# Kernel optimization log

Measured on AMD Instinct MI355X. Metric: run time of the kernel, lower is better.

## Reference

```python
import jax, jax.numpy as jnp
import numpy as np

N_NODES = 50000
N_EDGES = 800000
IN_DIM = 128
HIDDEN = 32
HEADS = 4
OUT_DIM = 40
NEG_SLOPE = 0.2


def _segment_softmax(logits, seg, num_segments):
    # logits: [E, H], seg: [E] destination node ids
    m = jax.ops.segment_max(logits, seg, num_segments=num_segments)  # [N, H]
    e = jnp.exp(logits - m[seg])
    s = jax.ops.segment_sum(e, seg, num_segments=num_segments)  # [N, H]
    return e / s[seg]


def _gat_conv(x, src, dst, W, a_src, a_dst, b, heads, out_ch, concat):
    N = x.shape[0]
    h = (x @ W).reshape(N, heads, out_ch)  # [N, H, C]
    alpha_src = jnp.einsum('nhc,hc->nh', h, a_src)  # [N, H]
    alpha_dst = jnp.einsum('nhc,hc->nh', h, a_dst)  # [N, H]
    logits = jax.nn.leaky_relu(alpha_src[src] + alpha_dst[dst], NEG_SLOPE)  # [E, H]
    alpha = _segment_softmax(logits, dst, N)  # [E, H]
    msg = h[src] * alpha[:, :, None]  # [E, H, C]
    out = jax.ops.segment_sum(msg, dst, num_segments=N)  # [N, H, C]
    if concat:
        out = out.reshape(N, heads * out_ch)
    else:
        out = out.mean(axis=1)
    return out + b


def setup_inputs() -> dict:
    key = jax.random.key(0)
    ks = jax.random.split(key, 12)
    x = jax.random.normal(ks[0], (N_NODES, IN_DIM), dtype=jnp.float32)
    edge_index = jax.random.randint(ks[1], (2, N_EDGES), 0, N_NODES, dtype=jnp.int64 if jax.config.read('jax_enable_x64') else jnp.int32)
    s1 = 1.0 / np.sqrt(IN_DIM)
    W1 = jax.random.uniform(ks[2], (IN_DIM, HEADS * HIDDEN), jnp.float32, -s1, s1)
    att_src1 = jax.random.uniform(ks[3], (HEADS, HIDDEN), jnp.float32, -1, 1) / np.sqrt(HIDDEN)
    att_dst1 = jax.random.uniform(ks[4], (HEADS, HIDDEN), jnp.float32, -1, 1) / np.sqrt(HIDDEN)
    b1 = jnp.zeros((HEADS * HIDDEN,), jnp.float32)
    s2 = 1.0 / np.sqrt(HEADS * HIDDEN)
    W2 = jax.random.uniform(ks[5], (HEADS * HIDDEN, OUT_DIM), jnp.float32, -s2, s2)
    att_src2 = jax.random.uniform(ks[6], (1, OUT_DIM), jnp.float32, -1, 1) / np.sqrt(OUT_DIM)
    att_dst2 = jax.random.uniform(ks[7], (1, OUT_DIM), jnp.float32, -1, 1) / np.sqrt(OUT_DIM)
    b2 = jnp.zeros((OUT_DIM,), jnp.float32)
    return {
        'x': x, 'edge_index': edge_index,
        'W1': W1, 'att_src1': att_src1, 'att_dst1': att_dst1, 'b1': b1,
        'W2': W2, 'att_src2': att_src2, 'att_dst2': att_dst2, 'b2': b2,
    }


def reference(x, edge_index, W1, att_src1, att_dst1, b1, W2, att_src2, att_dst2, b2):
    N = x.shape[0]
    # PyG GATConv default add_self_loops=True
    loop = jnp.arange(N, dtype=edge_index.dtype)
    src = jnp.concatenate([edge_index[0], loop])
    dst = jnp.concatenate([edge_index[1], loop])
    # dropout(p=0.6) is identity in eval mode
    h = _gat_conv(x, src, dst, W1, att_src1, att_dst1, b1, HEADS, HIDDEN, concat=True)
    h = jax.nn.relu(h)
    out = _gat_conv(h, src, dst, W2, att_src2, att_dst2, b2, 1, OUT_DIM, concat=True)
    return out
```

## Files before the change

kernel.cpp:

```cpp
#include <hip/hip_runtime.h>
#include <hip/hip_bf16.h>
#include <hip/hip_fp16.h>
#include <math.h>

#define N_NODES 50000
#define N_EDGES 800000
#define E_TOT   850000
#define IN_DIM  128
#define HID     32
#define HEADS   4
#define D1      128
#define OUT_DIM 40
#define H2P     64
#define NEG_SLOPE 0.2f

#define SCAN_TILE 1024
#define SCAN_NB   ((N_NODES + SCAN_TILE - 1) / SCAN_TILE)
#define G1_ROWS   64
#define GEMM1_NB  ((N_NODES + G1_ROWS - 1) / G1_ROWS)
#define CNT_NB    ((E_TOT + 255) / 256)
#define W2T_LD    132

__global__ __launch_bounds__(256) void gemm1_count(
    const float* __restrict__ x, const float* __restrict__ W,
    const float* __restrict__ as_v, const float* __restrict__ ad_v,
    __half* __restrict__ h1h, float* __restrict__ asrc, float* __restrict__ adst,
    const int* __restrict__ ei, int* __restrict__ deg)
{
  __shared__ float xs[G1_ROWS][IN_DIM];
  __shared__ float wbuf[2][8 * D1];
  const int t = threadIdx.x;
  if (blockIdx.x >= GEMM1_NB) {
    int e = (blockIdx.x - GEMM1_NB) * 256 + t;
    if (e < E_TOT) {
      int d = (e < N_EDGES) ? ei[N_EDGES + e] : e - N_EDGES;
      atomicAdd(deg + d, 1);
    }
    return;
  }
  const int nb = blockIdx.x * G1_ROWS;
  for (int i = t; i < G1_ROWS * (IN_DIM / 4); i += 256) {
    int r = i >> 5, k4 = (i & 31) * 4;
    int n = nb + r;
    float4 v = (n < N_NODES) ? *reinterpret_cast<const float4*>(x + (size_t)n * IN_DIM + k4)
                             : make_float4(0.f, 0.f, 0.f, 0.f);
    *reinterpret_cast<float4*>(&xs[r][k4]) = v;
  }
  float4 wreg = *reinterpret_cast<const float4*>(W + t * 4);
  *reinterpret_cast<float4*>(&wbuf[0][t * 4]) = wreg;
  __syncthreads();

  const int ct = t & 31, col0 = ct * 4;
  const int rt = t >> 5;
  float acc[8][4];
#pragma unroll
  for (int r = 0; r < 8; ++r)
#pragma unroll
    for (int c = 0; c < 4; ++c) acc[r][c] = 0.f;

  const int NK8 = IN_DIM / 8;
  for (int k8 = 0; k8 < NK8; ++k8) {
    const int cur = k8 & 1;
    if (k8 + 1 < NK8)
      wreg = *reinterpret_cast<const float4*>(W + (size_t)(k8 + 1) * 8 * D1 + t * 4);
#pragma unroll
    for (int half = 0; half < 2; ++half) {
      const int kb = k8 * 8 + half * 4;
      float4 xv[8];
#pragma unroll
      for (int r = 0; r < 8; ++r)
        xv[r] = *reinterpret_cast<const float4*>(&xs[rt * 8 + r][kb]);
      float4 wv[4];
#pragma unroll
      for (int kk = 0; kk < 4; ++kk)
        wv[kk] = *reinterpret_cast<const float4*>(&wbuf[cur][(half * 4 + kk) * D1 + col0]);
#pragma unroll
      for (int r = 0; r < 8; ++r) {
        acc[r][0] += xv[r].x * wv[0].x + xv[r].y * wv[1].x + xv[r].z * wv[2].x + xv[r].w * wv[3].x;
        acc[r][1] += xv[r].x * wv[0].y + xv[r].y * wv[1].y + xv[r].z * wv[2].y + xv[r].w * wv[3].y;
        acc[r][2] += xv[r].x * wv[0].z + xv[r].y * wv[1].z + xv[r].z * wv[2].z + xv[r].w * wv[3].z;
        acc[r][3] += xv[r].x * wv[0].w + xv[r].y * wv[1].w + xv[r].z * wv[2].w + xv[r].w * wv[3].w;
      }
    }
    if (k8 + 1 < NK8)
      *reinterpret_cast<float4*>(&wbuf[cur ^ 1][t * 4]) = wreg;
    __syncthreads();
  }

  const int head = col0 >> 5;
  const int cc0  = col0 & 31;
  const float4 asv = *reinterpret_cast<const float4*>(as_v + head * HID + cc0);
  const float4 adv = *reinterpret_cast<const float4*>(ad_v + head * HID + cc0);
#pragma unroll
  for (int r = 0; r < 8; ++r) {
    int n = nb + rt * 8 + r;
    bool ok = n < N_NODES;
    if (ok) {
      __half2 p0 = __floats2half2_rn(acc[r][0], acc[r][1]);
      __half2 p1 = __floats2half2_rn(acc[r][2], acc[r][3]);
      uint2 pk;
      pk.x = *reinterpret_cast<unsigned*>(&p0);
      pk.y = *reinterpret_cast<unsigned*>(&p1);
      *reinterpret_cast<uint2*>(h1h + (size_t)n * D1 + col0) = pk;
    }
    float cs = acc[r][0] * asv.x + acc[r][1] * asv.y + acc[r][2] * asv.z + acc[r][3] * asv.w;
    float cd = acc[r][0] * adv.x + acc[r][1] * adv.y + acc[r][2] * adv.z + acc[r][3] * adv.w;
#pragma unroll
    for (int off = 1; off < 8; off <<= 1) {
      cs += __shfl_xor(cs, off, 64);
      cd += __shfl_xor(cd, off, 64);
    }
    if ((ct & 7) == 0 && ok) {
      asrc[n * HEADS + head] = cs;
      adst[n * HEADS + head] = cd;
    }
  }
}

__global__ void zero_deg(int* __restrict__ deg)
{
  int i = blockIdx.x * blockDim.x + threadIdx.x;
  if (i < N_NODES) deg[i] = 0;
}

__global__ __launch_bounds__(256) void scan_p1(const int* __restrict__ deg,
                                               int* __restrict__ blocksum)
{
  int base = blockIdx.x * SCAN_TILE + threadIdx.x * 4;
  int s = 0;
#pragma unroll
  for (int i = 0; i < 4; ++i) {
    int idx = base + i;
    if (idx < N_NODES) s += deg[idx];
  }
#pragma unroll
  for (int off = 1; off < 64; off <<= 1) s += __shfl_xor(s, off, 64);
  __shared__ int ws[4];
  if ((threadIdx.x & 63) == 0) ws[threadIdx.x >> 6] = s;
  __syncthreads();
  if (threadIdx.x == 0) blocksum[blockIdx.x] = ws[0] + ws[1] + ws[2] + ws[3];
}

__global__ void scan_p2(const int* __restrict__ blocksum, int* __restrict__ blockoff,
                        int* __restrict__ row_off)
{
  int t = threadIdx.x;
  int v = (t < SCAN_NB) ? blocksum[t] : 0;
  int incl = v;
#pragma unroll
  for (int off = 1; off < 64; off <<= 1) {
    int u = __shfl_up(incl, off, 64);
    if (t >= off) incl += u;
  }
  if (t < SCAN_NB) blockoff[t] = incl - v;
  if (t == 0) row_off[N_NODES] = E_TOT;
}

__global__ __launch_bounds__(256) void scan_p3(const int* __restrict__ deg,
                                               const int* __restrict__ blockoff,
                                               int* __restrict__ row_off,
                                               int* __restrict__ cursor)
{
  const int t = threadIdx.x;
  const int lane = t & 63, wid = t >> 6;
  int base = blockIdx.x * SCAN_TILE + t * 4;
  int local[4]; int lsum = 0;
#pragma unroll
  for (int i = 0; i < 4; ++i) {
    int idx = base + i;
    local[i] = (idx < N_NODES) ? deg[idx] : 0;
    lsum += local[i];
  }
  int incl = lsum;
#pragma unroll
  for (int off = 1; off < 64; off <<= 1) {
    int u = __shfl_up(incl, off, 64);
    if (lane >= off) incl += u;
  }
  __shared__ int wtot[4];
  if (lane == 63) wtot[wid] = incl;
  __syncthreads();
  int wpre = 0;
  for (int w = 0; w < wid; ++w) wpre += wtot[w];
  int run = blockoff[blockIdx.x] + wpre + (incl - lsum);
#pragma unroll
  for (int i = 0; i < 4; ++i) {
    int idx = base + i;
    if (idx < N_NODES) { row_off[idx] = run; cursor[idx] = run; run += local[i]; }
  }
}

__global__ void scatter_csr(const int* __restrict__ ei, int* __restrict__ cursor,
                            int* __restrict__ csr_src)
{
  int e = blockIdx.x * blockDim.x + threadIdx.x;
  if (e >= E_TOT) return;
  int s, d;
  if (e < N_EDGES) { s = ei[e]; d = ei[N_EDGES + e]; }
  else             { s = d = e - N_EDGES; }
  int pos = atomicAdd(cursor + d, 1);
  csr_src[pos] = s;
}

__global__ __launch_bounds__(256) void agg1(
    const int* __restrict__ row_off, const int* __restrict__ csr_src,
    const float* __restrict__ asrc, const float* __restrict__ adst,
    const __half* __restrict__ h1h, const float* __restrict__ b1,
    float* __restrict__ lbuf, float* __restrict__ z)
{
  int n = blockIdx.x * 4 + (threadIdx.x >> 6);
  if (n >= N_NODES) return;
  const int lane = threadIdx.x & 63;
  const int start = row_off[n], end = row_off[n + 1];
  const int h = lane & 3;
  const float adst_h = adst[n * HEADS + h];
  float vmax = -1e30f;
  for (int i = start + (lane >> 2); i < end; i += 16)
    vmax = fmaxf(vmax, asrc[csr_src[i] * HEADS + h]);
#pragma unroll
  for (int off = 4; off < 64; off <<= 1)
    vmax = fmaxf(vmax, __shfl_xor(vmax, off, 64));
  float v = vmax + adst_h;
  const float mle = v > 0.f ? v : NEG_SLOPE * v;
  float ssum = 0.f;
  for (int i = start + (lane >> 2); i < end; i += 16) {
    float tv = asrc[csr_src[i] * HEADS + h] + adst_h;
    float le = tv > 0.f ? tv : NEG_SLOPE * tv;
    float e = __expf(le - mle);
    lbuf[(size_t)i * 4 + h] = e;
    ssum += e;
  }
#pragma unroll
  for (int off = 4; off < 64; off <<= 1)
    ssum += __shfl_xor(ssum, off, 64);
  const int hh = lane >> 4;
  const float inv = 1.f / __shfl(ssum, hh, 64);
  float2 acc = make_float2(0.f, 0.f);
  int i = start;
  for (; i + 8 <= end; i += 8) {
    float cc[8]; float2 vv[8];
#pragma unroll
    for (int u = 0; u < 8; ++u) {
      int s = csr_src[i + u];
      cc[u] = lbuf[(size_t)(i + u) * 4 + hh];
      vv[u] = __half22float2(*(reinterpret_cast<const __half2*>(h1h + (size_t)s * D1) + lane));
    }
#pragma unroll
    for (int u = 0; u < 8; ++u) {
      acc.x += cc[u] * vv[u].x;
      acc.y += cc[u] * vv[u].y;
    }
  }
  for (; i < end; ++i) {
    int s = csr_src[i];
    float c = lbuf[(size_t)i * 4 + hh];
    float2 hv = __half22float2(*(reinterpret_cast<const __half2*>(h1h + (size_t)s * D1) + lane));
    acc.x += c * hv.x;
    acc.y += c * hv.y;
  }
  float2 bb = *reinterpret_cast<const float2*>(b1 + 2 * lane);
  float r0 = acc.x * inv + bb.x;
  float r1 = acc.y * inv + bb.y;
  float2 o = make_float2(r0 > 0.f ? r0 : 0.f, r1 > 0.f ? r1 : 0.f);
  *reinterpret_cast<float2*>(z + (size_t)n * D1 + 2 * lane) = o;
}

__global__ __launch_bounds__(256) void gemm2(
    const float* __restrict__ z, const float* __restrict__ W2,
    const float* __restrict__ as2, const float* __restrict__ ad2,
    __half* __restrict__ h2h, float* __restrict__ asrc2, float* __restrict__ adst2)
{
  __shared__ float zs[32][IN_DIM];
  __shared__ float w2t[OUT_DIM][W2T_LD];
  const int nb = blockIdx.x * 32;
  const int t  = threadIdx.x;
  for (int i = t; i < 32 * (IN_DIM / 4); i += 256) {
    int r = i >> 5, k4 = (i & 31) * 4;
    int n = nb + r;
    float4 v = (n < N_NODES) ? *reinterpret_cast<const float4*>(z + (size_t)n * IN_DIM + k4)
                             : make_float4(0.f, 0.f, 0.f, 0.f);
    *reinterpret_cast<float4*>(&zs[r][k4]) = v;
  }
  for (int i = t; i < IN_DIM * OUT_DIM; i += 256) {
    int k = i / OUT_DIM, c = i - k * OUT_DIM;
    w2t[c][k] = W2[i];
  }
  __syncthreads();
  const int col = t & 63;
  const int rbase = (t >> 6) * 8;
  const bool valid = col < OUT_DIM;
  const int colc = valid ? col : (OUT_DIM - 1);
  float acc[8];
#pragma unroll
  for (int r = 0; r < 8; ++r) acc[r] = 0.f;
  for (int k = 0; k < IN_DIM; k += 4) {
    float4 wv = *reinterpret_cast<const float4*>(&w2t[colc][k]);
    float4 xv[8];
#pragma unroll
    for (int r = 0; r < 8; ++r)
      xv[r] = *reinterpret_cast<const float4*>(&zs[rbase + r][k]);
#pragma unroll
    for (int r = 0; r < 8; ++r)
      acc[r] += xv[r].x * wv.x + xv[r].y * wv.y + xv[r].z * wv.z + xv[r].w * wv.w;
  }
  const float a_s = valid ? as2[col] : 0.f;
  const float a_d = valid ? ad2[col] : 0.f;
#pragma unroll
  for (int r = 0; r < 8; ++r) {
    int n = nb + rbase + r;
    float cs = acc[r] * a_s, cd = acc[r] * a_d;
#pragma unroll
    for (int off = 32; off >= 1; off >>= 1) {
      cs += __shfl_xor(cs, off, 64);
      cd += __shfl_xor(cd, off, 64);
    }
    if (n < N_NODES) {
      if (valid) h2h[(size_t)n * H2P + col] = __float2half_rn(acc[r]);
      if (col == 0) { asrc2[n] = cs; adst2[n] = cd; }
    }
  }
}

__global__ __launch_bounds__(256) void agg2(
    const int* __restrict__ row_off, const int* __restrict__ csr_src,
    const float* __restrict__ asrc, const float* __restrict__ adst,
    const __half* __restrict__ h2h, const float* __restrict__ b2,
    float* __restrict__ lbuf, float* __restrict__ out)
{
  int n = blockIdx.x * 4 + (threadIdx.x >> 6);
  if (n >= N_NODES) return;
  const int lane = threadIdx.x & 63;
  const int start = row_off[n], end = row_off[n + 1];
  const float adstn = adst[n];
  float vmax = -1e30f;
  for (int i = start + lane; i < end; i += 64)
    vmax = fmaxf(vmax, asrc[csr_src[i]]);
#pragma unroll
  for (int off = 1; off < 64; off <<= 1)
    vmax = fmaxf(vmax, __shfl_xor(vmax, off, 64));
  float v = vmax + adstn;
  const float mle = v > 0.f ? v : NEG_SLOPE * v;
  float ssum = 0.f;
  for (int i = start + lane; i < end; i += 64) {
    float t = asrc[csr_src[i]] + adstn;
    float le = t > 0.f ? t : NEG_SLOPE * t;
    float e = __expf(le - mle);
    lbuf[i] = e;
    ssum += e;
  }
#pragma unroll
  for (int off = 1; off < 64; off <<= 1)
    ssum += __shfl_xor(ssum, off, 64);
  const float inv = 1.f / ssum;
  if (lane < OUT_DIM) {
    float acc = 0.f;
    int i = start;
    for (; i + 8 <= end; i += 8) {
      float cc[8]; float vv[8];
#pragma unroll
      for (int u = 0; u < 8; ++u) {
        cc[u] = lbuf[i + u];
        vv[u] = __half2float(h2h[(size_t)csr_src[i + u] * H2P + lane]);
      }
#pragma unroll
      for (int u = 0; u < 8; ++u) acc += cc[u] * vv[u];
    }
    for (; i < end; ++i)
      acc += lbuf[i] * __half2float(h2h[(size_t)csr_src[i] * H2P + lane]);
    out[(size_t)n * OUT_DIM + lane] = acc * inv + b2[lane];
  }
}

extern "C" void kernel_launch(void* const* d_in, const int* in_sizes, int n_in,
                              void* d_out, int out_size, void* d_ws, size_t ws_size,
                              hipStream_t stream)
{
  const float* x    = (const float*)d_in[0];
  const int*   ei   = (const int*)  d_in[1];
  const float* W1   = (const float*)d_in[2];
  const float* as1  = (const float*)d_in[3];
  const float* ad1  = (const float*)d_in[4];
  const float* b1   = (const float*)d_in[5];
  const float* W2   = (const float*)d_in[6];
  const float* as2  = (const float*)d_in[7];
  const float* ad2  = (const float*)d_in[8];
  const float* b2   = (const float*)d_in[9];
  float* out = (float*)d_out;

  float* ws = (float*)d_ws;
  __half* h1h  = (__half*)(ws + 0);
  __half* h2h  = (__half*)(ws + 0);
  float* z     = ws +  6400000;
  float* asrc1 = ws + 12800000;
  float* adst1 = ws + 13000000;
  float* asrc2 = ws + 13200000;
  float* adst2 = ws + 13250000;
  int* deg     = (int*)(ws + 13300000);
  int* row_off = (int*)(ws + 13350000);
  int* cursor  = (int*)(ws + 13410000);
  int* csr_src = (int*)(ws + 13460000);
  int* blocksum= (int*)(ws + 14320000);
  int* blockoff= (int*)(ws + 14320100);
  float* lbuf  = ws + 14400000;

  const int B = 256;
  zero_deg<<<(N_NODES + B - 1) / B, B, 0, stream>>>(deg);
  gemm1_count<<<GEMM1_NB + CNT_NB, B, 0, stream>>>(x, W1, as1, ad1, h1h, asrc1, adst1, ei, deg);
  scan_p1<<<SCAN_NB, B, 0, stream>>>(deg, blocksum);
  scan_p2<<<1, 64, 0, stream>>>(blocksum, blockoff, row_off);
  scan_p3<<<SCAN_NB, B, 0, stream>>>(deg, blockoff, row_off, cursor);
  scatter_csr<<<(E_TOT + B - 1) / B, B, 0, stream>>>(ei, cursor, csr_src);
  agg1<<<(N_NODES + 3) / 4, B, 0, stream>>>(row_off, csr_src, asrc1, adst1, h1h, b1, lbuf, z);
  gemm2<<<(N_NODES + 31) / 32, B, 0, stream>>>(z, W2, as2, ad2, h2h, asrc2, adst2);
  agg2<<<(N_NODES + 3) / 4, B, 0, stream>>>(row_off, csr_src, asrc2, adst2, h2h, b2, lbuf, out);
}
```

Before: 329.8 us.

## Use MFMA fp16 for first GEMM and keep softmax weights in LDS

Replaces the scalar-FMA first-layer GEMM with MFMA 16x16x32 fp16 instructions, using a pre-swizzled fp16 copy of W1 built in a new init kernel that also zeros degrees. The degree count now runs as a grid-stride loop inside the GEMM blocks. Both aggregation kernels keep per-edge softmax coefficients in shared memory when a node's degree fits a cap, falling back to the global buffer otherwise. This trades fp16 rounding of x inputs and extra LDS use for less FMA work and less global round-trip traffic.

```diff
diff --git a/kernel.cpp b/kernel.cpp
--- a/kernel.cpp
+++ b/kernel.cpp
@@ -13,114 +13,104 @@
 #define OUT_DIM 40
 #define H2P     64
 #define NEG_SLOPE 0.2f
+#define CAP     96
 
 #define SCAN_TILE 1024
 #define SCAN_NB   ((N_NODES + SCAN_TILE - 1) / SCAN_TILE)
-#define G1_ROWS   64
-#define GEMM1_NB  ((N_NODES + G1_ROWS - 1) / G1_ROWS)
-#define CNT_NB    ((E_TOT + 255) / 256)
+#define GEMM1_NB  ((N_NODES + 63) / 64)
 #define W2T_LD    132
 
-__global__ __launch_bounds__(256) void gemm1_count(
-    const float* __restrict__ x, const float* __restrict__ W,
+typedef _Float16 f16x8 __attribute__((ext_vector_type(8)));
+typedef float    f32x4 __attribute__((ext_vector_type(4)));
+
+__global__ __launch_bounds__(256) void init_wf_deg(
+    const float* __restrict__ W, _Float16* __restrict__ wf, int* __restrict__ deg)
+{
+  const int b = blockIdx.x, t = threadIdx.x;
+  if (b < 64) {
+    int tid = b * 256 + t;
+    int j = tid & 7, lane = (tid >> 3) & 63, nt = (tid >> 9) & 7, kc = tid >> 12;
+    int k = kc * 32 + ((lane >> 4) << 3) + j;
+    int n = nt * 16 + (lane & 15);
+    wf[tid] = (_Float16)W[k * D1 + n];
+  } else {
+    int i = (b - 64) * 256 + t;
+    if (i < N_NODES) deg[i] = 0;
+  }
+}
+
+__global__ __launch_bounds__(256) void gemm1_mfma_count(
+    const float* __restrict__ x, const _Float16* __restrict__ wf,
     const float* __restrict__ as_v, const float* __restrict__ ad_v,
-    __half* __restrict__ h1h, float* __restrict__ asrc, float* __restrict__ adst,
+    _Float16* __restrict__ h1h, float* __restrict__ asrc, float* __restrict__ adst,
     const int* __restrict__ ei, int* __restrict__ deg)
 {
-  __shared__ float xs[G1_ROWS][IN_DIM];
-  __shared__ float wbuf[2][8 * D1];
   const int t = threadIdx.x;
-  if (blockIdx.x >= GEMM1_NB) {
-    int e = (blockIdx.x - GEMM1_NB) * 256 + t;
-    if (e < E_TOT) {
-      int d = (e < N_EDGES) ? ei[N_EDGES + e] : e - N_EDGES;
-      atomicAdd(deg + d, 1);
-    }
-    return;
-  }
-  const int nb = blockIdx.x * G1_ROWS;
-  for (int i = t; i < G1_ROWS * (IN_DIM / 4); i += 256) {
-    int r = i >> 5, k4 = (i & 31) * 4;
-    int n = nb + r;
-    float4 v = (n < N_NODES) ? *reinterpret_cast<const float4*>(x + (size_t)n * IN_DIM + k4)
-                             : make_float4(0.f, 0.f, 0.f, 0.f);
-    *reinterpret_cast<float4*>(&xs[r][k4]) = v;
-  }
-  float4 wreg = *reinterpret_cast<const float4*>(W + t * 4);
-  *reinterpret_cast<float4*>(&wbuf[0][t * 4]) = wreg;
-  __syncthreads();
-
-  const int ct = t & 31, col0 = ct * 4;
-  const int rt = t >> 5;
-  float acc[8][4];
-#pragma unroll
-  for (int r = 0; r < 8; ++r)
-#pragma unroll
-    for (int c = 0; c < 4; ++c) acc[r][c] = 0.f;
-
-  const int NK8 = IN_DIM / 8;
-  for (int k8 = 0; k8 < NK8; ++k8) {
-    const int cur = k8 & 1;
-    if (k8 + 1 < NK8)
-      wreg = *reinterpret_cast<const float4*>(W + (size_t)(k8 + 1) * 8 * D1 + t * 4);
-#pragma unroll
-    for (int half = 0; half < 2; ++half) {
-      const int kb = k8 * 8 + half * 4;
-      float4 xv[8];
-#pragma unroll
-      for (int r = 0; r < 8; ++r)
-        xv[r] = *reinterpret_cast<const float4*>(&xs[rt * 8 + r][kb]);
-      float4 wv[4];
-#pragma unroll
-      for (int kk = 0; kk < 4; ++kk)
-        wv[kk] = *reinterpret_cast<const float4*>(&wbuf[cur][(half * 4 + kk) * D1 + col0]);
-#pragma unroll
-      for (int r = 0; r < 8; ++r) {
-        acc[r][0] += xv[r].x * wv[0].x + xv[r].y * wv[1].x + xv[r].z * wv[2].x + xv[r].w * wv[3].x;
-        acc[r][1] += xv[r].x * wv[0].y + xv[r].y * wv[1].y + xv[r].z * wv[2].y + xv[r].w * wv[3].y;
-        acc[r][2] += xv[r].x * wv[0].z + xv[r].y * wv[1].z + xv[r].z * wv[2].z + xv[r].w * wv[3].z;
-        acc[r][3] += xv[r].x * wv[0].w + xv[r].y * wv[1].w + xv[r].z * wv[2].w + xv[r].w * wv[3].w;
+  const int wave = t >> 6, lane = t & 63;
+  const int lr = lane & 15, lq = lane >> 4;
+  const int rowbase = blockIdx.x * 64 + wave * 16;
+  const int arow = rowbase + lr;
+
+  f32x4 acc[8];
+#pragma unroll
+  for (int nt = 0; nt < 8; ++nt) acc[nt] = (f32x4){0.f, 0.f, 0.f, 0.f};
+
+  const float* xrow = x + (size_t)arow * IN_DIM;
+  const f16x8* wfv = reinterpret_cast<const f16x8*>(wf);
+#pragma unroll
+  for (int kc = 0; kc < 4; ++kc) {
+    float4 lo = make_float4(0.f, 0.f, 0.f, 0.f), hi = lo;
+    if (arow < N_NODES) {
+      lo = *reinterpret_cast<const float4*>(xrow + kc * 32 + lq * 8);
+      hi = *reinterpret_cast<const float4*>(xrow + kc * 32 + lq * 8 + 4);
+    }
+    f16x8 a;
+    a[0] = (_Float16)lo.x; a[1] = (_Float16)lo.y; a[2] = (_Float16)lo.z; a[3] = (_Float16)lo.w;
+    a[4] = (_Float16)hi.x; a[5] = (_Float16)hi.y; a[6] = (_Float16)hi.z; a[7] = (_Float16)hi.w;
+    const f16x8* bbase = wfv + (size_t)(kc * 8) * 64 + lane;
+#pragma unroll
+    for (int nt = 0; nt < 8; ++nt) {
+      f16x8 bfrag = bbase[nt * 64];
+      acc[nt] = __builtin_amdgcn_mfma_f32_16x16x32_f16(a, bfrag, acc[nt], 0, 0, 0);
+    }
+  }
+
+  float as_lo[4], as_hi[4], ad_lo[4], ad_hi[4];
+#pragma unroll
+  for (int h = 0; h < 4; ++h) {
+    as_lo[h] = as_v[h * HID + lr];      ad_lo[h] = ad_v[h * HID + lr];
+    as_hi[h] = as_v[h * HID + 16 + lr]; ad_hi[h] = ad_v[h * HID + 16 + lr];
+  }
+#pragma unroll
+  for (int nt = 0; nt < 8; ++nt) {
+#pragma unroll
+    for (int r = 0; r < 4; ++r) {
+      int m = rowbase + lq * 4 + r;
+      if (m < N_NODES) h1h[(size_t)m * D1 + nt * 16 + lr] = (_Float16)acc[nt][r];
+    }
+  }
+#pragma unroll
+  for (int h = 0; h < 4; ++h) {
+#pragma unroll
+    for (int r = 0; r < 4; ++r) {
+      float ps = acc[2 * h][r] * as_lo[h] + acc[2 * h + 1][r] * as_hi[h];
+      float pd = acc[2 * h][r] * ad_lo[h] + acc[2 * h + 1][r] * ad_hi[h];
+#pragma unroll
+      for (int off = 1; off < 16; off <<= 1) {
+        ps += __shfl_xor(ps, off, 64);
+        pd += __shfl_xor(pd, off, 64);
       }
-    }
-    if (k8 + 1 < NK8)
-      *reinterpret_cast<float4*>(&wbuf[cur ^ 1][t * 4]) = wreg;
-    __syncthreads();
-  }
-
-  const int head = col0 >> 5;
-  const int cc0  = col0 & 31;
-  const float4 asv = *reinterpret_cast<const float4*>(as_v + head * HID + cc0);
-  const float4 adv = *reinterpret_cast<const float4*>(ad_v + head * HID + cc0);
-#pragma unroll
-  for (int r = 0; r < 8; ++r) {
-    int n = nb + rt * 8 + r;
-    bool ok = n < N_NODES;
-    if (ok) {
-      __half2 p0 = __floats2half2_rn(acc[r][0], acc[r][1]);
-      __half2 p1 = __floats2half2_rn(acc[r][2], acc[r][3]);
-      uint2 pk;
-      pk.x = *reinterpret_cast<unsigned*>(&p0);
-      pk.y = *reinterpret_cast<unsigned*>(&p1);
-      *reinterpret_cast<uint2*>(h1h + (size_t)n * D1 + col0) = pk;
-    }
-    float cs = acc[r][0] * asv.x + acc[r][1] * asv.y + acc[r][2] * asv.z + acc[r][3] * asv.w;
-    float cd = acc[r][0] * adv.x + acc[r][1] * adv.y + acc[r][2] * adv.z + acc[r][3] * adv.w;
-#pragma unroll
-    for (int off = 1; off < 8; off <<= 1) {
-      cs += __shfl_xor(cs, off, 64);
-      cd += __shfl_xor(cd, off, 64);
-    }
-    if ((ct & 7) == 0 && ok) {
-      asrc[n * HEADS + head] = cs;
-      adst[n * HEADS + head] = cd;
-    }
-  }
-}
-
-__global__ void zero_deg(int* __restrict__ deg)
-{
-  int i = blockIdx.x * blockDim.x + threadIdx.x;
-  if (i < N_NODES) deg[i] = 0;
+      int m = rowbase + lq * 4 + r;
+      if (lr == 0 && m < N_NODES) {
+        asrc[m * HEADS + h] = ps;
+        adst[m * HEADS + h] = pd;
+      }
+    }
+  }
+  for (int e = blockIdx.x * 256 + t; e < E_TOT; e += gridDim.x * 256) {
+    int d = (e < N_EDGES) ? ei[N_EDGES + e] : e - N_EDGES;
+    atomicAdd(deg + d, 1);
+  }
 }
 
 __global__ __launch_bounds__(256) void scan_p1(const int* __restrict__ deg,
@@ -208,10 +198,14 @@
     const __half* __restrict__ h1h, const float* __restrict__ b1,
     float* __restrict__ lbuf, float* __restrict__ z)
 {
-  int n = blockIdx.x * 4 + (threadIdx.x >> 6);
+  __shared__ float cbuf[4][CAP * 4];
+  const int w = threadIdx.x >> 6;
+  int n = blockIdx.x * 4 + w;
   if (n >= N_NODES) return;
   const int lane = threadIdx.x & 63;
   const int start = row_off[n], end = row_off[n + 1];
+  const bool useL = (end - start) <= CAP;
+  float* cb = cbuf[w];
   const int h = lane & 3;
   const float adst_h = adst[n * HEADS + h];
   float vmax = -1e30f;
@@ -227,7 +221,8 @@
     float tv = asrc[csr_src[i] * HEADS + h] + adst_h;
     float le = tv > 0.f ? tv : NEG_SLOPE * tv;
     float e = __expf(le - mle);
-    lbuf[(size_t)i * 4 + h] = e;
+    if (useL) cb[(i - start) * 4 + h] = e;
+    else      lbuf[(size_t)i * 4 + h] = e;
     ssum += e;
   }
 #pragma unroll
@@ -236,27 +231,37 @@
   const int hh = lane >> 4;
   const float inv = 1.f / __shfl(ssum, hh, 64);
   float2 acc = make_float2(0.f, 0.f);
-  int i = start;
-  for (; i + 8 <= end; i += 8) {
-    float cc[8]; float2 vv[8];
-#pragma unroll
-    for (int u = 0; u < 8; ++u) {
-      int s = csr_src[i + u];
-      cc[u] = lbuf[(size_t)(i + u) * 4 + hh];
-      vv[u] = __half22float2(*(reinterpret_cast<const __half2*>(h1h + (size_t)s * D1) + lane));
-    }
-#pragma unroll
-    for (int u = 0; u < 8; ++u) {
-      acc.x += cc[u] * vv[u].x;
-      acc.y += cc[u] * vv[u].y;
-    }
-  }
-  for (; i < end; ++i) {
-    int s = csr_src[i];
-    float c = lbuf[(size_t)i * 4 + hh];
-    float2 hv = __half22float2(*(reinterpret_cast<const __half2*>(h1h + (size_t)s * D1) + lane));
-    acc.x += c * hv.x;
-    acc.y += c * hv.y;
+  if (useL) {
+    int i = start;
+    for (; i + 8 <= end; i += 8) {
+      float cc[8]; float2 vv[8];
+#pragma unroll
+      for (int u = 0; u < 8; ++u) {
+        int s = csr_src[i + u];
+        cc[u] = cb[(i + u - start) * 4 + hh];
+        vv[u] = __half22float2(*(reinterpret_cast<const __half2*>(h1h + (size_t)s * D1) + lane));
+      }
+#pragma unroll
+      for (int u = 0; u < 8; ++u) {
+        acc.x += cc[u] * vv[u].x;
+        acc.y += cc[u] * vv[u].y;
+      }
+    }
+    for (; i < end; ++i) {
+      int s = csr_src[i];
+      float c = cb[(i - start) * 4 + hh];
+      float2 hv = __half22float2(*(reinterpret_cast<const __half2*>(h1h + (size_t)s * D1) + lane));
+      acc.x += c * hv.x;
+      acc.y += c * hv.y;
+    }
+  } else {
+    for (int i = start; i < end; ++i) {
+      int s = csr_src[i];
+      float c = lbuf[(size_t)i * 4 + hh];
+      float2 hv = __half22float2(*(reinterpret_cast<const __half2*>(h1h + (size_t)s * D1) + lane));
+      acc.x += c * hv.x;
+      acc.y += c * hv.y;
+    }
   }
   float2 bb = *reinterpret_cast<const float2*>(b1 + 2 * lane);
   float r0 = acc.x * inv + bb.x;
@@ -327,10 +332,14 @@
     const __half* __restrict__ h2h, const float* __restrict__ b2,
     float* __restrict__ lbuf, float* __restrict__ out)
 {
-  int n = blockIdx.x * 4 + (threadIdx.x >> 6);
+  __shared__ float cbuf[4][CAP];
+  const int w = threadIdx.x >> 6;
+  int n = blockIdx.x * 4 + w;
   if (n >= N_NODES) return;
   const int lane = threadIdx.x & 63;
   const int start = row_off[n], end = row_off[n + 1];
+  const bool useL = (end - start) <= CAP;
+  float* cb = cbuf[w];
   const float adstn = adst[n];
   float vmax = -1e30f;
   for (int i = start + lane; i < end; i += 64)
@@ -345,7 +354,8 @@
     float t = asrc[csr_src[i]] + adstn;
     float le = t > 0.f ? t : NEG_SLOPE * t;
     float e = __expf(le - mle);
-    lbuf[i] = e;
+    if (useL) cb[i - start] = e;
+    else      lbuf[i] = e;
     ssum += e;
   }
 #pragma unroll
@@ -354,19 +364,24 @@
   const float inv = 1.f / ssum;
   if (lane < OUT_DIM) {
     float acc = 0.f;
-    int i = start;
-    for (; i + 8 <= end; i += 8) {
-      float cc[8]; float vv[8];
-#pragma unroll
-      for (int u = 0; u < 8; ++u) {
-        cc[u] = lbuf[i + u];
-        vv[u] = __half2float(h2h[(size_t)csr_src[i + u] * H2P + lane]);
+    if (useL) {
+      int i = start;
+      for (; i + 8 <= end; i += 8) {
+        float cc[8]; float vv[8];
+#pragma unroll
+        for (int u = 0; u < 8; ++u) {
+          cc[u] = cb[i + u - start];
+          vv[u] = __half2float(h2h[(size_t)csr_src[i + u] * H2P + lane]);
+        }
+#pragma unroll
+        for (int u = 0; u < 8; ++u) acc += cc[u] * vv[u];
       }
-#pragma unroll
-      for (int u = 0; u < 8; ++u) acc += cc[u] * vv[u];
-    }
-    for (; i < end; ++i)
-      acc += lbuf[i] * __half2float(h2h[(size_t)csr_src[i] * H2P + lane]);
+      for (; i < end; ++i)
+        acc += cb[i - start] * __half2float(h2h[(size_t)csr_src[i] * H2P + lane]);
+    } else {
+      for (int i = start; i < end; ++i)
+        acc += lbuf[i] * __half2float(h2h[(size_t)csr_src[i] * H2P + lane]);
+    }
     out[(size_t)n * OUT_DIM + lane] = acc * inv + b2[lane];
   }
 }
@@ -388,8 +403,8 @@
   float* out = (float*)d_out;
 
   float* ws = (float*)d_ws;
-  __half* h1h  = (__half*)(ws + 0);
-  __half* h2h  = (__half*)(ws + 0);
+  _Float16* h1h = (_Float16*)(ws + 0);
+  __half*   h2h = (__half*)(ws + 0);
   float* z     = ws +  6400000;
   float* asrc1 = ws + 12800000;
   float* adst1 = ws + 13000000;
@@ -402,15 +417,17 @@
   int* blocksum= (int*)(ws + 14320000);
   int* blockoff= (int*)(ws + 14320100);
   float* lbuf  = ws + 14400000;
+  _Float16* wf = (_Float16*)(ws + 17800000);
 
   const int B = 256;
-  zero_deg<<<(N_NODES + B - 1) / B, B, 0, stream>>>(deg);
-  gemm1_count<<<GEMM1_NB + CNT_NB, B, 0, stream>>>(x, W1, as1, ad1, h1h, asrc1, adst1, ei, deg);
+  init_wf_deg<<<64 + (N_NODES + B - 1) / B, B, 0, stream>>>(W1, wf, deg);
+  gemm1_mfma_count<<<GEMM1_NB, B, 0, stream>>>(x, wf, as1, ad1, h1h, asrc1, adst1, ei, deg);
   scan_p1<<<SCAN_NB, B, 0, stream>>>(deg, blocksum);
   scan_p2<<<1, 64, 0, stream>>>(blocksum, blockoff, row_off);
   scan_p3<<<SCAN_NB, B, 0, stream>>>(deg, blockoff, row_off, cursor);
   scatter_csr<<<(E_TOT + B - 1) / B, B, 0, stream>>>(ei, cursor, csr_src);
-  agg1<<<(N_NODES + 3) / 4, B, 0, stream>>>(row_off, csr_src, asrc1, adst1, h1h, b1, lbuf, z);
+  agg1<<<(N_NODES + 3) / 4, B, 0, stream>>>(row_off, csr_src, asrc1, adst1,
+                                            (const __half*)h1h, b1, lbuf, z);
   gemm2<<<(N_NODES + 31) / 32, B, 0, stream>>>(z, W2, as2, ad2, h2h, asrc2, adst2);
   agg2<<<(N_NODES + 3) / 4, B, 0, stream>>>(row_off, csr_src, asrc2, adst2, h2h, b2, lbuf, out);
 }
```

Result: faster. 319.2 us (-3.2%).
